# Optimization experiments

Hardware: AMD Instinct MI355X
Metric: run time of the kernel (lower is better)

## Reference

```python
import jax, jax.numpy as jnp
import numpy as np

H = 70  # LSTM hidden size (hard-coded in module)

def _lstm_cell(x, h, c, Wih, Whh, bih, bhh):
    # torch gate order: i, f, g, o
    gates = x @ Wih.T + h @ Whh.T + bih + bhh  # [B, 4H]
    i, f, g, o = jnp.split(gates, 4, axis=-1)
    i = jax.nn.sigmoid(i); f = jax.nn.sigmoid(f)
    g = jnp.tanh(g);       o = jax.nn.sigmoid(o)
    c_new = f * c + i * g
    h_new = o * jnp.tanh(c_new)
    return h_new, c_new

def setup_inputs() -> dict:
    key = jax.random.key(0)
    ks = jax.random.split(key, 16)
    T, B, D = 512, 4096, 64
    s_in = 1.0 / np.sqrt(H)
    def u(k, shape):
        return jax.random.uniform(k, shape, jnp.float32, -s_in, s_in)
    return {
        "data_in": jax.random.normal(ks[0], (T, B, D), jnp.float32),
        "batch_dim": B,
        "W_ih0": u(ks[1], (4 * H, D)),  "W_hh0": u(ks[2], (4 * H, H)),
        "b_ih0": u(ks[3], (4 * H,)),    "b_hh0": u(ks[4], (4 * H,)),
        "W_ih1": u(ks[5], (4 * H, H)),  "W_hh1": u(ks[6], (4 * H, H)),
        "b_ih1": u(ks[7], (4 * H,)),    "b_hh1": u(ks[8], (4 * H,)),
        "W1": u(ks[9], (50, H)), "b1": u(ks[10], (50,)),
        "W2": u(ks[11], (1, 50)), "b2": u(ks[12], (1,)),
    }

def reference(data_in, batch_dim, W_ih0, W_hh0, b_ih0, b_hh0,
              W_ih1, W_hh1, b_ih1, b_hh1, W1, b1, W2, b2):
    B = data_in.shape[1]
    z = jnp.zeros((B, H), data_in.dtype)
    def step(carry, x_t):
        h0, c0, h1, c1 = carry
        h0, c0 = _lstm_cell(x_t, h0, c0, W_ih0, W_hh0, b_ih0, b_hh0)
        h1, c1 = _lstm_cell(h0, h1, c1, W_ih1, W_hh1, b_ih1, b_hh1)
        return (h0, c0, h1, c1), None
    (h0, c0, h1, c1), _ = jax.lax.scan(step, (z, z, z, z), data_in)
    # head uses h_n of the last (second) layer
    out = jax.nn.relu(h1 @ W1.T + b1)
    out = jax.nn.sigmoid(out @ W2.T + b2)  # [B, 1]
    return out
```

## Files before the change

kernel.cpp:

```cpp
#include <hip/hip_runtime.h>
#include <stdint.h>

#define T_STEPS 512
#define BATCH   4096
#define DIN     64
#define HID     70
#define KDIM    160
#define KS      5
#define RB      16
#define WAVES   12
#define NTHR    (WAVES*64)
#define PROWS   384

typedef __bf16 bf16x8 __attribute__((ext_vector_type(8)));
typedef float  f32x4  __attribute__((ext_vector_type(4)));
typedef unsigned short ushort_t;
typedef ushort_t us4 __attribute__((ext_vector_type(4)));

__device__ __forceinline__ ushort_t f2bf(float f) {
    uint32_t u = __float_as_uint(f);
    u += 0x7fffu + ((u >> 16) & 1u);
    return (ushort_t)(u >> 16);
}
__device__ __forceinline__ float sigm(float x) {
    return __builtin_amdgcn_rcpf(1.0f + __expf(-x));
}
__device__ __forceinline__ float tanh_(float x) {
    float r = __builtin_amdgcn_rcpf(1.0f + __expf(2.0f * x));
    return 1.0f - 2.0f * r;
}

__global__ void prep_kernel(const float* __restrict__ Wih0, const float* __restrict__ Whh0,
                            const float* __restrict__ bih0, const float* __restrict__ bhh0,
                            const float* __restrict__ Wih1, const float* __restrict__ Whh1,
                            const float* __restrict__ bih1, const float* __restrict__ bhh1,
                            ushort_t* __restrict__ W0p, ushort_t* __restrict__ W1p,
                            float* __restrict__ bsum0, float* __restrict__ bsum1) {
    int idx = blockIdx.x * 256 + threadIdx.x;
    const int n = PROWS * KDIM;
    if (idx < n) {
        int p = idx / KDIM, k = idx - p * KDIM;
        int nt = p >> 4, n15 = p & 15;
        int w = nt % 6, j = nt / 6;
        int h = 6 * n15 + w;
        float v0 = 0.f, v1 = 0.f;
        if (h < HID) {
            int g = j * HID + h;
            if (k < 64)        v0 = Wih0[g*64 + k];
            else if (k < 134)  v0 = Whh0[g*70 + (k-64)];
            if (k < 70)                  v1 = Wih1[g*70 + k];
            else if (k >= 80 && k < 150) v1 = Whh1[g*70 + (k-80)];
        }
        W0p[idx] = f2bf(v0);
        W1p[idx] = f2bf(v1);
    }
    if (idx < 280) {
        bsum0[idx] = bih0[idx] + bhh0[idx];
        bsum1[idx] = bih1[idx] + bhh1[idx];
    }
}

__global__ __launch_bounds__(NTHR) void lstm_kernel(
    const float* __restrict__ x,
    const ushort_t* __restrict__ W0p, const ushort_t* __restrict__ W1p,
    const float* __restrict__ bsum0, const float* __restrict__ bsum1,
    const float* __restrict__ W1h, const float* __restrict__ b1h,
    const float* __restrict__ W2h, const float* __restrict__ b2h,
    float* __restrict__ out)
{
    constexpr int AS = 168;
    __shared__ alignas(16) ushort_t A0[2][RB*AS];
    __shared__ alignas(16) ushort_t A1[2][RB*AS];
    __shared__ float h1f[RB*HID];
    __shared__ float mid[RB*50];

    const int tid  = threadIdx.x;
    const int wave = tid >> 6;
    const int lane = tid & 63;
    const int n15  = lane & 15;
    const int q    = lane >> 4;
    const int blk  = blockIdx.x;
    const bool isL0 = (wave >= 6);
    const int lw   = isL0 ? wave - 6 : wave;
    const int h    = 6*n15 + lw;
    const bool active = (h < HID);

    const ushort_t* __restrict__ Wp = isL0 ? W0p : W1p;
    const float*    __restrict__ bs = isL0 ? bsum0 : bsum1;
    bf16x8 wf[4][KS];
    float  wb[4];
    #pragma unroll
    for (int j = 0; j < 4; j++) {
        const int base = ((lw + 6*j)*16 + n15)*KDIM + q*8;
        #pragma unroll
        for (int ks = 0; ks < KS; ks++)
            wf[j][ks] = *(const bf16x8*)(Wp + base + ks*32);
        wb[j] = active ? bs[j*HID + h] : 0.f;
    }

    for (int i = tid; i < RB*AS; i += NTHR) {
        A0[0][i] = 0; A0[1][i] = 0; A1[0][i] = 0; A1[1][i] = 0;
    }

    const int  xt   = tid - 384;
    const bool xl   = (xt >= 0) && (xt < 256);
    const int  xrow = xt >> 4;
    const int  xcol = (xt & 15) * 4;
    const float* xptr = x + ((size_t)blk*RB + xrow)*DIN + xcol;

    f32x4 x0v, x1v, xcur;
    if (xl) {
        x0v  = *(const f32x4*)(xptr);
        x1v  = *(const f32x4*)(xptr + (size_t)1*(BATCH*DIN));
        xcur = *(const f32x4*)(xptr + (size_t)2*(BATCH*DIN));
    }
    __syncthreads();
    if (xl) {
        us4 s0, s1;
        #pragma unroll
        for (int e = 0; e < 4; e++) { s0[e] = f2bf(x0v[e]); s1[e] = f2bf(x1v[e]); }
        *(us4*)(&A0[1][xrow*AS + xcol]) = s0;
        *(us4*)(&A0[0][xrow*AS + xcol]) = s1;
    }
    __syncthreads();

    float cc[4] = {0,0,0,0};

    if (isL0) {
        bf16x8 a[KS];
        #pragma unroll
        for (int ks = 0; ks < KS; ks++)
            a[ks] = *(const bf16x8*)(&A0[1][n15*AS + ks*32 + q*8]);
        f32x4 gi = {wb[0],wb[0],wb[0],wb[0]};
        f32x4 gf = {wb[1],wb[1],wb[1],wb[1]};
        f32x4 gg = {wb[2],wb[2],wb[2],wb[2]};
        f32x4 go = {wb[3],wb[3],wb[3],wb[3]};
        #pragma unroll
        for (int ks = 0; ks < KS; ks++) {
            gi = __builtin_amdgcn_mfma_f32_16x16x32_bf16(a[ks], wf[0][ks], gi, 0,0,0);
            gf = __builtin_amdgcn_mfma_f32_16x16x32_bf16(a[ks], wf[1][ks], gf, 0,0,0);
            gg = __builtin_amdgcn_mfma_f32_16x16x32_bf16(a[ks], wf[2][ks], gg, 0,0,0);
            go = __builtin_amdgcn_mfma_f32_16x16x32_bf16(a[ks], wf[3][ks], go, 0,0,0);
        }
        if (active) {
            #pragma unroll
            for (int r = 0; r < 4; r++) {
                float i_ = sigm(gi[r]), f_ = sigm(gf[r]);
                float g_ = tanh_(gg[r]), o_ = sigm(go[r]);
                float cn = f_*cc[r] + i_*g_;
                cc[r] = cn;
                ushort_t hb = f2bf(o_*tanh_(cn));
                const int row = q*4 + r;
                A1[0][row*AS + h]      = hb;
                A0[0][row*AS + 64 + h] = hb;
            }
        }
    }
    __syncthreads();

    for (int p = 0; p < T_STEPS; p++) {
        const int cur = p & 1, nxt = cur ^ 1;
        f32x4 xn;
        if (xl) {
            const int tn = (p+3 < T_STEPS) ? p+3 : T_STEPS-1;
            xn = *(const f32x4*)(xptr + (size_t)tn*(BATCH*DIN));
        }
        const ushort_t* __restrict__ Apan = isL0 ? &A0[cur][0] : &A1[cur][0];
        bf16x8 a[KS];
        #pragma unroll
        for (int ks = 0; ks < KS; ks++)
            a[ks] = *(const bf16x8*)(Apan + n15*AS + ks*32 + q*8);
        f32x4 gi = {wb[0],wb[0],wb[0],wb[0]};
        f32x4 gf = {wb[1],wb[1],wb[1],wb[1]};
        f32x4 gg = {wb[2],wb[2],wb[2],wb[2]};
        f32x4 go = {wb[3],wb[3],wb[3],wb[3]};
        #pragma unroll
        for (int ks = 0; ks < KS; ks++) {
            gi = __builtin_amdgcn_mfma_f32_16x16x32_bf16(a[ks], wf[0][ks], gi, 0,0,0);
            gf = __builtin_amdgcn_mfma_f32_16x16x32_bf16(a[ks], wf[1][ks], gf, 0,0,0);
            gg = __builtin_amdgcn_mfma_f32_16x16x32_bf16(a[ks], wf[2][ks], gg, 0,0,0);
            go = __builtin_amdgcn_mfma_f32_16x16x32_bf16(a[ks], wf[3][ks], go, 0,0,0);
        }
        if (xl) {
            us4 s;
            #pragma unroll
            for (int e = 0; e < 4; e++) s[e] = f2bf(xcur[e]);
            *(us4*)(&A0[nxt][xrow*AS + xcol]) = s;
        }
        if (active) {
            #pragma unroll
            for (int r = 0; r < 4; r++) {
                float i_ = sigm(gi[r]), f_ = sigm(gf[r]);
                float g_ = tanh_(gg[r]), o_ = sigm(go[r]);
                float cn = f_*cc[r] + i_*g_;
                cc[r] = cn;
                float hv = o_*tanh_(cn);
                const int row = q*4 + r;
                if (isL0) {
                    ushort_t hb = f2bf(hv);
                    A1[nxt][row*AS + h]      = hb;
                    A0[nxt][row*AS + 64 + h] = hb;
                } else {
                    A1[nxt][row*AS + 80 + h] = f2bf(hv);
                    if (p == T_STEPS-1) h1f[row*HID + h] = hv;
                }
            }
        }
        if (xl) xcur = xn;
        __syncthreads();
    }

    for (int uu = tid; uu < RB*50; uu += NTHR) {
        const int r = uu / 50, j = uu - r*50;
        float s = b1h[j];
        const float* wgt = W1h + j*HID;
        const float* hh  = h1f + r*HID;
        #pragma unroll 7
        for (int k = 0; k < HID; k++) s += wgt[k]*hh[k];
        mid[uu] = fmaxf(s, 0.0f);
    }
    __syncthreads();
    if (tid < RB) {
        float s = b2h[0];
        const float* m = mid + tid*50;
        #pragma unroll 10
        for (int j = 0; j < 50; j++) s += W2h[j]*m[j];
        out[blk*RB + tid] = sigm(s);
    }
}

extern "C" void kernel_launch(void* const* d_in, const int* in_sizes, int n_in,
                              void* d_out, int out_size, void* d_ws, size_t ws_size,
                              hipStream_t stream) {
    (void)in_sizes; (void)n_in; (void)out_size; (void)ws_size;
    const float* x    = (const float*)d_in[0];
    const float* Wih0 = (const float*)d_in[2];
    const float* Whh0 = (const float*)d_in[3];
    const float* bih0 = (const float*)d_in[4];
    const float* bhh0 = (const float*)d_in[5];
    const float* Wih1 = (const float*)d_in[6];
    const float* Whh1 = (const float*)d_in[7];
    const float* bih1 = (const float*)d_in[8];
    const float* bhh1 = (const float*)d_in[9];
    const float* W1h  = (const float*)d_in[10];
    const float* b1h  = (const float*)d_in[11];
    const float* W2h  = (const float*)d_in[12];
    const float* b2h  = (const float*)d_in[13];

    char* ws = (char*)d_ws;
    ushort_t* W0p  = (ushort_t*)ws;
    ushort_t* W1p  = (ushort_t*)(ws + 122880);
    float*    bs0  = (float*)(ws + 245760);
    float*    bs1  = (float*)(ws + 245760 + 1120);

    prep_kernel<<<240, 256, 0, stream>>>(Wih0, Whh0, bih0, bhh0,
                                         Wih1, Whh1, bih1, bhh1,
                                         W0p, W1p, bs0, bs1);
    lstm_kernel<<<BATCH/RB, NTHR, 0, stream>>>(x, W0p, W1p, bs0, bs1,
                                               W1h, b1h, W2h, b2h, (float*)d_out);
}
```

Measured before the change: 1.284 ms.

## Interleave gates per hidden unit, transpose MFMA, fold exp scaling into weights

The weight packing is reordered so each 16-row MFMA tile holds the four gates of four hidden units. The MFMA is transposed (weights as A, state as B), so each lane gets all four gates of one unit in one accumulator. This cuts the padded gate tiles from 24 to 18, which means 15 MFMAs per wave per step instead of 20. The -log2e and 2log2e scales are folded into the weights and biases in prep, so the cell computes the gates with exp2 and fused reciprocals, and the two layer panels are merged into one shared buffer. The risk is extra exp2 overflow clamping and bf16 rounding of the pre-scaled weights.

After: 1.037 ms. 19.2% less time.

```diff
diff --git a/kernel.cpp b/kernel.cpp
--- a/kernel.cpp
+++ b/kernel.cpp
@@ -10,13 +10,18 @@
 #define RB      16
 #define WAVES   12
 #define NTHR    (WAVES*64)
-#define PROWS   384
+#define NTILES  18
+#define CH      3
+#define ASP     232
 
 typedef __bf16 bf16x8 __attribute__((ext_vector_type(8)));
 typedef float  f32x4  __attribute__((ext_vector_type(4)));
 typedef unsigned short ushort_t;
 typedef ushort_t us4 __attribute__((ext_vector_type(4)));
 
+#define NLOG2E   (-1.44269504088896340736f)
+#define TWOLOG2E ( 2.88539008177792681472f)
+
 __device__ __forceinline__ ushort_t f2bf(float f) {
     uint32_t u = __float_as_uint(f);
     u += 0x7fffu + ((u >> 16) & 1u);
@@ -25,9 +30,18 @@
 __device__ __forceinline__ float sigm(float x) {
     return __builtin_amdgcn_rcpf(1.0f + __expf(-x));
 }
-__device__ __forceinline__ float tanh_(float x) {
-    float r = __builtin_amdgcn_rcpf(1.0f + __expf(2.0f * x));
-    return 1.0f - 2.0f * r;
+
+__device__ __forceinline__ float cell(const f32x4 a, float& cc) {
+    float u0 = __builtin_amdgcn_exp2f(a[0]);
+    float u1 = __builtin_amdgcn_exp2f(a[1]);
+    float v  = __builtin_amdgcn_exp2f(fminf(a[2], 88.0f));
+    float u3 = __builtin_amdgcn_exp2f(a[3]);
+    float ig = (v - 1.0f) * __builtin_amdgcn_rcpf((1.0f + u0) * (1.0f + v));
+    float f_ = __builtin_amdgcn_rcpf(1.0f + u1);
+    float cn = fmaf(f_, cc, ig);
+    cc = cn;
+    float w  = __builtin_amdgcn_exp2f(fminf(cn * TWOLOG2E, 88.0f));
+    return (w - 1.0f) * __builtin_amdgcn_rcpf((1.0f + u3) * (1.0f + w));
 }
 
 __global__ void prep_kernel(const float* __restrict__ Wih0, const float* __restrict__ Whh0,
@@ -35,42 +49,48 @@
                             const float* __restrict__ Wih1, const float* __restrict__ Whh1,
                             const float* __restrict__ bih1, const float* __restrict__ bhh1,
                             ushort_t* __restrict__ W0p, ushort_t* __restrict__ W1p,
-                            float* __restrict__ bsum0, float* __restrict__ bsum1) {
+                            float* __restrict__ B0p, float* __restrict__ B1p) {
     int idx = blockIdx.x * 256 + threadIdx.x;
-    const int n = PROWS * KDIM;
+    const int n = NTILES * 16 * KDIM;
     if (idx < n) {
-        int p = idx / KDIM, k = idx - p * KDIM;
-        int nt = p >> 4, n15 = p & 15;
-        int w = nt % 6, j = nt / 6;
-        int h = 6 * n15 + w;
+        int row = idx / KDIM, k = idx - row * KDIM;
+        int t = row >> 4, m = row & 15;
+        int gate = m & 3, h = 4*t + (m >> 2);
+        float sc = (gate == 2) ? TWOLOG2E : NLOG2E;
         float v0 = 0.f, v1 = 0.f;
         if (h < HID) {
-            int g = j * HID + h;
+            int g = gate * HID + h;
             if (k < 64)        v0 = Wih0[g*64 + k];
-            else if (k < 134)  v0 = Whh0[g*70 + (k-64)];
-            if (k < 70)                  v1 = Wih1[g*70 + k];
-            else if (k >= 80 && k < 150) v1 = Whh1[g*70 + (k-80)];
-        }
-        W0p[idx] = f2bf(v0);
-        W1p[idx] = f2bf(v1);
-    }
-    if (idx < 280) {
-        bsum0[idx] = bih0[idx] + bhh0[idx];
-        bsum1[idx] = bih1[idx] + bhh1[idx];
+            else if (k < 134)  v0 = Whh0[g*HID + (k - 64)];
+            if (k < 70)                   v1 = Wih1[g*HID + k];
+            else if (k >= 80 && k < 150)  v1 = Whh1[g*HID + (k - 80)];
+        }
+        W0p[idx] = f2bf(sc * v0);
+        W1p[idx] = f2bf(sc * v1);
+    }
+    if (idx < NTILES*16) {
+        int t = idx >> 4, m = idx & 15;
+        int gate = m & 3, h = 4*t + (m >> 2);
+        float sc = (gate == 2) ? TWOLOG2E : NLOG2E;
+        float s0 = 0.f, s1 = 0.f;
+        if (h < HID) {
+            int g = gate * HID + h;
+            s0 = sc * (bih0[g] + bhh0[g]);
+            s1 = sc * (bih1[g] + bhh1[g]);
+        }
+        B0p[idx] = s0; B1p[idx] = s1;
     }
 }
 
 __global__ __launch_bounds__(NTHR) void lstm_kernel(
     const float* __restrict__ x,
     const ushort_t* __restrict__ W0p, const ushort_t* __restrict__ W1p,
-    const float* __restrict__ bsum0, const float* __restrict__ bsum1,
+    const float* __restrict__ B0p, const float* __restrict__ B1p,
     const float* __restrict__ W1h, const float* __restrict__ b1h,
     const float* __restrict__ W2h, const float* __restrict__ b2h,
     float* __restrict__ out)
 {
-    constexpr int AS = 168;
-    __shared__ alignas(16) ushort_t A0[2][RB*AS];
-    __shared__ alignas(16) ushort_t A1[2][RB*AS];
+    __shared__ alignas(16) ushort_t P[2][RB*ASP];
     __shared__ float h1f[RB*HID];
     __shared__ float mid[RB*50];
 
@@ -82,25 +102,26 @@
     const int blk  = blockIdx.x;
     const bool isL0 = (wave >= 6);
     const int lw   = isL0 ? wave - 6 : wave;
-    const int h    = 6*n15 + lw;
-    const bool active = (h < HID);
+    const int t0   = lw * CH;
 
     const ushort_t* __restrict__ Wp = isL0 ? W0p : W1p;
-    const float*    __restrict__ bs = isL0 ? bsum0 : bsum1;
-    bf16x8 wf[4][KS];
-    float  wb[4];
+    const float*    __restrict__ Bp = isL0 ? B0p : B1p;
+
+    bf16x8 wA[CH][KS];
+    f32x4  bias[CH];
+    int    col[CH];
     #pragma unroll
-    for (int j = 0; j < 4; j++) {
-        const int base = ((lw + 6*j)*16 + n15)*KDIM + q*8;
+    for (int c = 0; c < CH; c++) {
+        const int rowb = ((t0 + c)*16 + n15)*KDIM + q*8;
         #pragma unroll
         for (int ks = 0; ks < KS; ks++)
-            wf[j][ks] = *(const bf16x8*)(Wp + base + ks*32);
-        wb[j] = active ? bs[j*HID + h] : 0.f;
-    }
-
-    for (int i = tid; i < RB*AS; i += NTHR) {
-        A0[0][i] = 0; A0[1][i] = 0; A1[0][i] = 0; A1[1][i] = 0;
-    }
+            wA[c][ks] = *(const bf16x8*)(Wp + rowb + ks*32);
+        bias[c] = *(const f32x4*)(Bp + (t0 + c)*16 + q*4);
+        col[c]  = (t0 + c)*4 + q;
+    }
+    const int kbase = (isL0 ? 0 : 64) + n15*ASP + q*8;
+
+    for (int i = tid; i < 2*RB*ASP; i += NTHR) (&P[0][0])[i] = 0;
 
     const int  xt   = tid - 384;
     const bool xl   = (xt >= 0) && (xt < 256);
@@ -119,41 +140,31 @@
         us4 s0, s1;
         #pragma unroll
         for (int e = 0; e < 4; e++) { s0[e] = f2bf(x0v[e]); s1[e] = f2bf(x1v[e]); }
-        *(us4*)(&A0[1][xrow*AS + xcol]) = s0;
-        *(us4*)(&A0[0][xrow*AS + xcol]) = s1;
-    }
-    __syncthreads();
-
-    float cc[4] = {0,0,0,0};
+        *(us4*)(&P[1][xrow*ASP + xcol]) = s0;
+        *(us4*)(&P[0][xrow*ASP + xcol]) = s1;
+    }
+    __syncthreads();
+
+    float cc[CH] = {0.f, 0.f, 0.f};
 
     if (isL0) {
-        bf16x8 a[KS];
+        bf16x8 b[KS];
         #pragma unroll
         for (int ks = 0; ks < KS; ks++)
-            a[ks] = *(const bf16x8*)(&A0[1][n15*AS + ks*32 + q*8]);
-        f32x4 gi = {wb[0],wb[0],wb[0],wb[0]};
-        f32x4 gf = {wb[1],wb[1],wb[1],wb[1]};
-        f32x4 gg = {wb[2],wb[2],wb[2],wb[2]};
-        f32x4 go = {wb[3],wb[3],wb[3],wb[3]};
+            b[ks] = *(const bf16x8*)(&P[1][kbase + ks*32]);
+        f32x4 acc[CH];
+        #pragma unroll
+        for (int c = 0; c < CH; c++) acc[c] = bias[c];
         #pragma unroll
         for (int ks = 0; ks < KS; ks++) {
-            gi = __builtin_amdgcn_mfma_f32_16x16x32_bf16(a[ks], wf[0][ks], gi, 0,0,0);
-            gf = __builtin_amdgcn_mfma_f32_16x16x32_bf16(a[ks], wf[1][ks], gf, 0,0,0);
-            gg = __builtin_amdgcn_mfma_f32_16x16x32_bf16(a[ks], wf[2][ks], gg, 0,0,0);
-            go = __builtin_amdgcn_mfma_f32_16x16x32_bf16(a[ks], wf[3][ks], go, 0,0,0);
-        }
-        if (active) {
             #pragma unroll
-            for (int r = 0; r < 4; r++) {
-                float i_ = sigm(gi[r]), f_ = sigm(gf[r]);
-                float g_ = tanh_(gg[r]), o_ = sigm(go[r]);
-                float cn = f_*cc[r] + i_*g_;
-                cc[r] = cn;
-                ushort_t hb = f2bf(o_*tanh_(cn));
-                const int row = q*4 + r;
-                A1[0][row*AS + h]      = hb;
-                A0[0][row*AS + 64 + h] = hb;
-            }
+            for (int c = 0; c < CH; c++)
+                acc[c] = __builtin_amdgcn_mfma_f32_16x16x32_bf16(wA[c][ks], b[ks], acc[c], 0,0,0);
+        }
+        #pragma unroll
+        for (int c = 0; c < CH; c++) {
+            float hv = cell(acc[c], cc[c]);
+            P[0][n15*ASP + 64 + col[c]] = f2bf(hv);
         }
     }
     __syncthreads();
@@ -165,45 +176,34 @@
             const int tn = (p+3 < T_STEPS) ? p+3 : T_STEPS-1;
             xn = *(const f32x4*)(xptr + (size_t)tn*(BATCH*DIN));
         }
-        const ushort_t* __restrict__ Apan = isL0 ? &A0[cur][0] : &A1[cur][0];
-        bf16x8 a[KS];
+        bf16x8 b[KS];
         #pragma unroll
         for (int ks = 0; ks < KS; ks++)
-            a[ks] = *(const bf16x8*)(Apan + n15*AS + ks*32 + q*8);
-        f32x4 gi = {wb[0],wb[0],wb[0],wb[0]};
-        f32x4 gf = {wb[1],wb[1],wb[1],wb[1]};
-        f32x4 gg = {wb[2],wb[2],wb[2],wb[2]};
-        f32x4 go = {wb[3],wb[3],wb[3],wb[3]};
+            b[ks] = *(const bf16x8*)(&P[cur][kbase + ks*32]);
+        f32x4 acc[CH];
+        #pragma unroll
+        for (int c = 0; c < CH; c++) acc[c] = bias[c];
         #pragma unroll
         for (int ks = 0; ks < KS; ks++) {
-            gi = __builtin_amdgcn_mfma_f32_16x16x32_bf16(a[ks], wf[0][ks], gi, 0,0,0);
-            gf = __builtin_amdgcn_mfma_f32_16x16x32_bf16(a[ks], wf[1][ks], gf, 0,0,0);
-            gg = __builtin_amdgcn_mfma_f32_16x16x32_bf16(a[ks], wf[2][ks], gg, 0,0,0);
-            go = __builtin_amdgcn_mfma_f32_16x16x32_bf16(a[ks], wf[3][ks], go, 0,0,0);
+            #pragma unroll
+            for (int c = 0; c < CH; c++)
+                acc[c] = __builtin_amdgcn_mfma_f32_16x16x32_bf16(wA[c][ks], b[ks], acc[c], 0,0,0);
         }
         if (xl) {
             us4 s;
             #pragma unroll
             for (int e = 0; e < 4; e++) s[e] = f2bf(xcur[e]);
-            *(us4*)(&A0[nxt][xrow*AS + xcol]) = s;
-        }
-        if (active) {
-            #pragma unroll
-            for (int r = 0; r < 4; r++) {
-                float i_ = sigm(gi[r]), f_ = sigm(gf[r]);
-                float g_ = tanh_(gg[r]), o_ = sigm(go[r]);
-                float cn = f_*cc[r] + i_*g_;
-                cc[r] = cn;
-                float hv = o_*tanh_(cn);
-                const int row = q*4 + r;
-                if (isL0) {
-                    ushort_t hb = f2bf(hv);
-                    A1[nxt][row*AS + h]      = hb;
-                    A0[nxt][row*AS + 64 + h] = hb;
-                } else {
-                    A1[nxt][row*AS + 80 + h] = f2bf(hv);
-                    if (p == T_STEPS-1) h1f[row*HID + h] = hv;
-                }
+            *(us4*)(&P[nxt][xrow*ASP + xcol]) = s;
+        }
+        #pragma unroll
+        for (int c = 0; c < CH; c++) {
+            float hv = cell(acc[c], cc[c]);
+            ushort_t hb = f2bf(hv);
+            if (isL0) {
+                P[nxt][n15*ASP + 64 + col[c]] = hb;
+            } else {
+                P[nxt][n15*ASP + 144 + col[c]] = hb;
+                if (p == T_STEPS-1 && col[c] < HID) h1f[n15*HID + col[c]] = hv;
             }
         }
         if (xl) xcur = xn;
@@ -248,14 +248,14 @@
     const float* b2h  = (const float*)d_in[13];
 
     char* ws = (char*)d_ws;
-    ushort_t* W0p  = (ushort_t*)ws;
-    ushort_t* W1p  = (ushort_t*)(ws + 122880);
-    float*    bs0  = (float*)(ws + 245760);
-    float*    bs1  = (float*)(ws + 245760 + 1120);
-
-    prep_kernel<<<240, 256, 0, stream>>>(Wih0, Whh0, bih0, bhh0,
+    ushort_t* W0p = (ushort_t*)ws;
+    ushort_t* W1p = (ushort_t*)(ws + 92160);
+    float*    B0p = (float*)(ws + 184320);
+    float*    B1p = (float*)(ws + 185472);
+
+    prep_kernel<<<180, 256, 0, stream>>>(Wih0, Whh0, bih0, bhh0,
                                          Wih1, Whh1, bih1, bhh1,
-                                         W0p, W1p, bs0, bs1);
-    lstm_kernel<<<BATCH/RB, NTHR, 0, stream>>>(x, W0p, W1p, bs0, bs1,
+                                         W0p, W1p, B0p, B1p);
+    lstm_kernel<<<BATCH/RB, NTHR, 0, stream>>>(x, W0p, W1p, B0p, B1p,
                                                W1h, b1h, W2h, b2h, (float*)d_out);
 }
```
